# Optimization experiments

Hardware: AMD Instinct MI355X
Metric: run time of the kernel (lower is better)

Reference implementation:

```python
import jax, jax.numpy as jnp
import numpy as np

N = 100000      # nodes
E = 1600000     # edges (avg degree 16)
NFEAT = 16
HID = 64
OUT = 4
K = 3           # TAGConv hops
L = 4           # number of TAGConv layers


def setup_inputs() -> dict:
    key = jax.random.key(0)
    ks = jax.random.split(key, 6)
    x = jax.random.normal(ks[0], (N, NFEAT), dtype=jnp.float32)
    edge_index = jax.random.randint(ks[1], (2, E), 0, N, dtype=jnp.int64)
    # TAGConv has one (bias-free) linear per hop k=0..K, plus a per-layer bias.
    W0 = jax.random.normal(ks[2], (K + 1, NFEAT, HID), dtype=jnp.float32) * 0.1
    b0 = jnp.zeros((HID,), dtype=jnp.float32)
    Wh = jax.random.normal(ks[3], (L - 1, K + 1, HID, HID), dtype=jnp.float32) * 0.1
    bh = jnp.zeros((L - 1, HID), dtype=jnp.float32)
    fcW = jax.random.normal(ks[4], (HID, OUT), dtype=jnp.float32) * 0.1
    fcb = jnp.zeros((OUT,), dtype=jnp.float32)
    return dict(x=x, edge_index=edge_index, W0=W0, b0=b0, Wh=Wh, bh=bh, fcW=fcW, fcb=fcb)


def _gcn_norm(src, dst, num_nodes):
    # symmetric GCN normalization, no self-loops (PyG TAGConv default)
    ones = jnp.ones(src.shape, dtype=jnp.float32)
    deg = jax.ops.segment_sum(ones, dst, num_segments=num_nodes)
    dinv = jnp.where(deg > 0, 1.0 / jnp.sqrt(jnp.maximum(deg, 1e-12)), 0.0)
    return dinv[src] * dinv[dst]  # [E]


def _tag_conv(x, src, dst, norm, W, b):
    # out = sum_{k=0..K} (A_norm^k x) W_k + b
    out = x @ W[0]
    h = x
    for k in range(1, W.shape[0]):
        h = jax.ops.segment_sum(norm[:, None] * h[src], dst, num_segments=x.shape[0])
        out = out + h @ W[k]
    return out + b


def reference(x, edge_index, W0, b0, Wh, bh, fcW, fcb):
    src, dst = edge_index[0], edge_index[1]
    norm = _gcn_norm(src, dst, x.shape[0])
    h = jax.nn.relu(_tag_conv(x, src, dst, norm, W0, b0))  # conv0 (+relu, dropout=identity)
    for l in range(Wh.shape[0] - 1):  # middle convs with relu
        h = jax.nn.relu(_tag_conv(h, src, dst, norm, Wh[l], bh[l]))
    h = _tag_conv(h, src, dst, norm, Wh[-1], bh[-1])  # last conv, no relu
    return h @ fcW + fcb  # [N, OUT]
```

## Files before the change

kernel.cpp:

```cpp
#include <hip/hip_runtime.h>
#include <hip/hip_fp16.h>

constexpr int Nn   = 100000;
constexpr int Ne   = 1600000;
constexpr int NF   = 16;
constexpr int HID  = 64;
constexpr int NOUT = 4;

constexpr int NBUK  = 391;
constexpr int CHUNK = 2048;
constexpr int NB1   = (Ne + CHUNK - 1) / CHUNK;
constexpr int NS    = NBUK * NB1;
constexpr int STASH = 6144;

union H8 { float4 f4; __half h[8]; };
union H4 { float2 f2; __half h[4]; };

typedef _Float16 f16x8 __attribute__((ext_vector_type(8)));
typedef float    f32x4 __attribute__((ext_vector_type(4)));


__global__ __launch_bounds__(256) void bhist_kernel(const int* __restrict__ dst,
                                                    int* __restrict__ ghist) {
    __shared__ int h[NBUK];
    int t = threadIdx.x;
    int b = blockIdx.x;
    for (int i = t; i < NBUK; i += 256) h[i] = 0;
    __syncthreads();
    int e0 = b * CHUNK;
    int e1 = (e0 + CHUNK < Ne) ? e0 + CHUNK : Ne;
    for (int e = e0 + t; e < e1; e += 256) atomicAdd(&h[dst[e] >> 8], 1);
    __syncthreads();
    for (int i = t; i < NBUK; i += 256) ghist[i * NB1 + b] = h[i];
}

__global__ __launch_bounds__(256) void scan1g_kernel(int* __restrict__ g,
                                                     int* __restrict__ bsum) {
    __shared__ int lds[256];
    int t = threadIdx.x;
    int base = blockIdx.x * 1024 + t * 4;
    int v0 = (base + 0 < NS) ? g[base + 0] : 0;
    int v1 = (base + 1 < NS) ? g[base + 1] : 0;
    int v2 = (base + 2 < NS) ? g[base + 2] : 0;
    int v3 = (base + 3 < NS) ? g[base + 3] : 0;
    lds[t] = v0 + v1 + v2 + v3;
    __syncthreads();
    for (int off = 1; off < 256; off <<= 1) {
        int a = lds[t];
        int b = (t >= off) ? lds[t - off] : 0;
        __syncthreads();
        lds[t] = a + b;
        __syncthreads();
    }
    int excl = (t > 0) ? lds[t - 1] : 0;
    if (base + 0 < NS) g[base + 0] = excl;
    if (base + 1 < NS) g[base + 1] = excl + v0;
    if (base + 2 < NS) g[base + 2] = excl + v0 + v1;
    if (base + 3 < NS) g[base + 3] = excl + v0 + v1 + v2;
    if (t == 255) bsum[blockIdx.x] = lds[255];
}

__global__ __launch_bounds__(512) void scan2g_kernel(int* __restrict__ bsum, int nb) {
    __shared__ int lds[512];
    int t = threadIdx.x;
    int v = (t < nb) ? bsum[t] : 0;
    lds[t] = v;
    __syncthreads();
    for (int off = 1; off < 512; off <<= 1) {
        int a = lds[t];
        int b = (t >= off) ? lds[t - off] : 0;
        __syncthreads();
        lds[t] = a + b;
        __syncthreads();
    }
    if (t < nb) bsum[t] = lds[t] - v;
}

__global__ __launch_bounds__(256) void scan3g_kernel(int* __restrict__ g,
                                                     const int* __restrict__ bsum) {
    int i = blockIdx.x * 256 + threadIdx.x;
    if (i < NS) g[i] += bsum[i >> 10];
}

__global__ __launch_bounds__(256) void bscatter_kernel(const int* __restrict__ src,
                                                       const int* __restrict__ dst,
                                                       const int* __restrict__ ghist,
                                                       int2* __restrict__ tmp) {
    __shared__ int hb[NBUK];
    __shared__ int cur[NBUK];
    int t = threadIdx.x;
    int b = blockIdx.x;
    for (int i = t; i < NBUK; i += 256) {
        hb[i] = ghist[i * NB1 + b];
        cur[i] = 0;
    }
    __syncthreads();
    int e0 = b * CHUNK;
    int e1 = (e0 + CHUNK < Ne) ? e0 + CHUNK : Ne;
    for (int e = e0 + t; e < e1; e += 256) {
        int d = dst[e];
        int s = src[e];
        int bin = d >> 8;
        int r = atomicAdd(&cur[bin], 1);
        tmp[hb[bin] + r] = make_int2(s, d);
    }
}

__global__ __launch_bounds__(256) void bcsr_kernel(const int2* __restrict__ tmp,
                                                   const int* __restrict__ ghist,
                                                   int* __restrict__ rowptr,
                                                   float* __restrict__ dinv,
                                                   int* __restrict__ colsrc) {
    __shared__ int2 stash[STASH];
    __shared__ int h[256];
    __shared__ int hs[256];
    __shared__ int cur[256];
    int t = threadIdx.x;
    int b = blockIdx.x;
    int lo = ghist[b * NB1];
    int hi = (b < NBUK - 1) ? ghist[(b + 1) * NB1] : Ne;
    int sz = hi - lo;
    h[t] = 0;
    cur[t] = 0;
    __syncthreads();
    for (int i = t; i < sz; i += 256) {
        int2 rec = tmp[lo + i];
        if (i < STASH) stash[i] = rec;
        atomicAdd(&h[rec.y & 255], 1);
    }
    __syncthreads();
    int myh = h[t];
    hs[t] = myh;
    __syncthreads();
    for (int off = 1; off < 256; off <<= 1) {
        int a = hs[t];
        int bb = (t >= off) ? hs[t - off] : 0;
        __syncthreads();
        hs[t] = a + bb;
        __syncthreads();
    }
    int excl = hs[t] - myh;
    __syncthreads();
    hs[t] = excl;
    int d = (b << 8) + t;
    if (d < Nn) {
        rowptr[d] = lo + excl;
        dinv[d] = (myh > 0) ? rsqrtf((float)myh) : 0.0f;
    }
    if (b == NBUK - 1 && t == 0) rowptr[Nn] = Ne;
    __syncthreads();
    for (int i = t; i < sz; i += 256) {
        int2 rec = (i < STASH) ? stash[i] : tmp[lo + i];
        int bin = rec.y & 255;
        int r = atomicAdd(&cur[bin], 1);
        colsrc[lo + hs[bin] + r] = rec.x;
    }
}

__global__ __launch_bounds__(256) void fill_kernel(const int* __restrict__ colsrc,
                                                   const float* __restrict__ dinv,
                                                   int2* __restrict__ edge2) {
    int e = blockIdx.x * 256 + threadIdx.x;
    if (e < Ne) {
        int s = colsrc[e];
        edge2[e] = make_int2(s, __float_as_int(dinv[s]));
    }
}

__global__ __launch_bounds__(256) void xcvt_kernel(const float* __restrict__ x,
                                                   __half* __restrict__ xh) {
    int i = blockIdx.x * 256 + threadIdx.x;
    if (i < Nn * NF / 4) {
        float4 v = reinterpret_cast<const float4*>(x)[i];
        H4 o;
        o.h[0] = __float2half(v.x);
        o.h[1] = __float2half(v.y);
        o.h[2] = __float2half(v.z);
        o.h[3] = __float2half(v.w);
        reinterpret_cast<float2*>(xh)[i] = o.f2;
    }
}


__global__ __launch_bounds__(256) void pull64h_kernel(const __half* __restrict__ hin,
                                                      const int* __restrict__ rowptr,
                                                      const int2* __restrict__ edge2,
                                                      const float* __restrict__ dinv,
                                                      __half* __restrict__ hout) {
    int lane = threadIdx.x & 63;
    int q  = lane & 3;
    int eo = (lane >> 2) & 3;
    int g  = lane >> 4;
    int n = blockIdx.x * 16 + (threadIdx.x >> 6) * 4 + g;
    if (n >= Nn) return;
    int r0 = rowptr[n];
    int r1 = rowptr[n + 1];
    float a[16];
#pragma unroll
    for (int j = 0; j < 16; ++j) a[j] = 0.f;

    int e = r0 + eo;
    int2 ed0 = (e < r1) ? edge2[e] : make_int2(0, 0);
    int2 ed1 = (e + 4 < r1) ? edge2[e + 4] : make_int2(0, 0);
    const float4* rp0 = reinterpret_cast<const float4*>(hin + (size_t)ed0.x * 64 + q * 16);
    float4 ga = rp0[0], gb = rp0[1];
#pragma unroll 1
    for (; e < r1; e += 4) {
        int2 ed2 = (e + 8 < r1) ? edge2[e + 8] : make_int2(0, 0);
        const float4* rp1 = reinterpret_cast<const float4*>(hin + (size_t)ed1.x * 64 + q * 16);
        float4 na = rp1[0], nb = rp1[1];
        float w = __int_as_float(ed0.y);
        H8 u0, u1;
        u0.f4 = ga;
        u1.f4 = gb;
#pragma unroll
        for (int j = 0; j < 8; ++j) a[j] += w * __half2float(u0.h[j]);
#pragma unroll
        for (int j = 0; j < 8; ++j) a[8 + j] += w * __half2float(u1.h[j]);
        ed0 = ed1; ed1 = ed2; ga = na; gb = nb;
    }
#pragma unroll
    for (int off = 4; off <= 8; off <<= 1)
#pragma unroll
        for (int j = 0; j < 16; ++j) a[j] += __shfl_xor(a[j], off);
    if (eo == 0) {
        float dn = dinv[n];
        H8 o0, o1;
#pragma unroll
        for (int j = 0; j < 8; ++j) o0.h[j] = __float2half(a[j] * dn);
#pragma unroll
        for (int j = 0; j < 8; ++j) o1.h[j] = __float2half(a[8 + j] * dn);
        float4* op = reinterpret_cast<float4*>(hout + (size_t)n * 64 + q * 16);
        op[0] = o0.f4;
        op[1] = o1.f4;
    }
}

__global__ __launch_bounds__(256) void pull16h_kernel(const __half* __restrict__ hin,
                                                      const int* __restrict__ rowptr,
                                                      const int2* __restrict__ edge2,
                                                      const float* __restrict__ dinv,
                                                      __half* __restrict__ hout) {
    int lane = threadIdx.x & 63;
    int q  = lane & 1;
    int eo = (lane >> 1) & 3;
    int g  = lane >> 3;
    int n = blockIdx.x * 32 + (threadIdx.x >> 6) * 8 + g;
    if (n >= Nn) return;
    int r0 = rowptr[n];
    int r1 = rowptr[n + 1];
    float a[8];
#pragma unroll
    for (int j = 0; j < 8; ++j) a[j] = 0.f;

    int e = r0 + eo;
    int2 ed0 = (e < r1) ? edge2[e] : make_int2(0, 0);
    int2 ed1 = (e + 4 < r1) ? edge2[e + 4] : make_int2(0, 0);
    float4 ga = *reinterpret_cast<const float4*>(hin + (size_t)ed0.x * 16 + q * 8);
#pragma unroll 1
    for (; e < r1; e += 4) {
        int2 ed2 = (e + 8 < r1) ? edge2[e + 8] : make_int2(0, 0);
        float4 na = *reinterpret_cast<const float4*>(hin + (size_t)ed1.x * 16 + q * 8);
        float w = __int_as_float(ed0.y);
        H8 u;
        u.f4 = ga;
#pragma unroll
        for (int j = 0; j < 8; ++j) a[j] += w * __half2float(u.h[j]);
        ed0 = ed1; ed1 = ed2; ga = na;
    }
#pragma unroll
    for (int off = 2; off <= 4; off <<= 1)
#pragma unroll
        for (int j = 0; j < 8; ++j) a[j] += __shfl_xor(a[j], off);
    if (eo == 0) {
        float dn = dinv[n];
        H8 o;
#pragma unroll
        for (int j = 0; j < 8; ++j) o.h[j] = __float2half(a[j] * dn);
        *reinterpret_cast<float4*>(hout + (size_t)n * 16 + q * 8) = o.f4;
    }
}

template <int ADDBIAS>
__global__ __launch_bounds__(256) void pull4_kernel(const float* __restrict__ uin,
                                                    const float* __restrict__ gadd,
                                                    const int* __restrict__ rowptr,
                                                    const int2* __restrict__ edge2,
                                                    const float* __restrict__ dinv,
                                                    const float* __restrict__ beff,
                                                    float* __restrict__ out) {
    int lane = threadIdx.x & 63;
    int eo = lane & 15;
    int n = blockIdx.x * 16 + ((threadIdx.x >> 6) << 2) + (lane >> 4);
    if (n >= Nn) return;
    int r0 = rowptr[n];
    int r1 = rowptr[n + 1];
    float ax = 0.f, ay = 0.f, az = 0.f, aw = 0.f;

    int e = r0 + eo;
    int2 ed0 = (e < r1) ? edge2[e] : make_int2(0, 0);
    int2 ed1 = (e + 16 < r1) ? edge2[e + 16] : make_int2(0, 0);
    float4 ga = *reinterpret_cast<const float4*>(uin + (size_t)ed0.x * 4);
#pragma unroll 1
    for (; e < r1; e += 16) {
        int2 ed2 = (e + 32 < r1) ? edge2[e + 32] : make_int2(0, 0);
        float4 na = *reinterpret_cast<const float4*>(uin + (size_t)ed1.x * 4);
        float w = __int_as_float(ed0.y);
        ax += w * ga.x;
        ay += w * ga.y;
        az += w * ga.z;
        aw += w * ga.w;
        ed0 = ed1; ed1 = ed2; ga = na;
    }
#pragma unroll
    for (int off = 1; off < 16; off <<= 1) {
        ax += __shfl_xor(ax, off);
        ay += __shfl_xor(ay, off);
        az += __shfl_xor(az, off);
        aw += __shfl_xor(aw, off);
    }
    if (eo == 0) {
        float dn = dinv[n];
        float4 g = *reinterpret_cast<const float4*>(gadd + (size_t)n * 4);
        float4 o;
        o.x = g.x + dn * ax;
        o.y = g.y + dn * ay;
        o.z = g.z + dn * az;
        o.w = g.w + dn * aw;
        if (ADDBIAS) {
            o.x += beff[0]; o.y += beff[1]; o.z += beff[2]; o.w += beff[3];
        }
        *reinterpret_cast<float4*>(out + (size_t)n * 4) = o;
    }
}

template <int KS>
__global__ __launch_bounds__(256) void wfrag_kernel(const float* __restrict__ W,
                                                    __half* __restrict__ Wfrag) {
    constexpr int NT = (4 * KS / 32) * 4 * 64;
    int tid = blockIdx.x * 256 + threadIdx.x;
    if (tid >= NT) return;
    int l  = tid & 63;
    int ct = (tid >> 6) & 3;
    int ks = tid >> 8;
    int c  = ct * 16 + (l & 15);
    int kb = ks * 32 + (l >> 4) * 8;
    H8 o;
#pragma unroll
    for (int j = 0; j < 8; ++j) {
        int k = kb + j;
        o.h[j] = __float2half(W[(size_t)(k / KS) * KS * 64 + (size_t)(k % KS) * 64 + c]);
    }
    *reinterpret_cast<float4*>(Wfrag + (size_t)tid * 8) = o.f4;
}

template <int KS, int RELU>
__global__ __launch_bounds__(256) void gemm4m_kernel(const __half* __restrict__ S0,
                                                     const __half* __restrict__ S1,
                                                     const __half* __restrict__ S2,
                                                     const __half* __restrict__ S3,
                                                     const __half* __restrict__ Wfrag,
                                                     const float* __restrict__ bias,
                                                     __half* __restrict__ out) {
    constexpr int NKS = 4 * KS / 32;
    int lane = threadIdx.x & 63;
    int wv = threadIdx.x >> 6;
    int base = blockIdx.x * 128 + wv * 32;
    int r = lane & 15;
    int qa = lane >> 4;
    int acol = qa * 8;
    const __half* Ss[4] = {S0, S1, S2, S3};
    f32x4 acc[2][4] = {};
    int row0 = base + r;       if (row0 >= Nn) row0 = Nn - 1;
    int row1 = base + 16 + r;  if (row1 >= Nn) row1 = Nn - 1;
#pragma unroll
    for (int ks = 0; ks < NKS; ++ks) {
        int k0 = ks * 32 + acol;
        const __half* Sa = Ss[k0 / KS];
        int col = k0 % KS;
        f16x8 a0 = *reinterpret_cast<const f16x8*>(Sa + (size_t)row0 * KS + col);
        f16x8 a1 = *reinterpret_cast<const f16x8*>(Sa + (size_t)row1 * KS + col);
        const __half* wp = Wfrag + ((size_t)(ks * 4) * 64 + lane) * 8;
#pragma unroll
        for (int ct = 0; ct < 4; ++ct) {
            f16x8 b = *reinterpret_cast<const f16x8*>(wp + (size_t)ct * 64 * 8);
            acc[0][ct] = __builtin_amdgcn_mfma_f32_16x16x32_f16(a0, b, acc[0][ct], 0, 0, 0);
            acc[1][ct] = __builtin_amdgcn_mfma_f32_16x16x32_f16(a1, b, acc[1][ct], 0, 0, 0);
        }
    }
    int ccol = lane & 15;
    int rb = (lane >> 4) * 4;
#pragma unroll
    for (int rt = 0; rt < 2; ++rt) {
#pragma unroll
        for (int ct = 0; ct < 4; ++ct) {
            float bi = bias[ct * 16 + ccol];
#pragma unroll
            for (int i = 0; i < 4; ++i) {
                int row = base + rt * 16 + rb + i;
                if (row < Nn) {
                    float v = acc[rt][ct][i] + bi;
                    if (RELU) v = fmaxf(v, 0.f);
                    out[(size_t)row * 64 + ct * 16 + ccol] = __float2half(v);
                }
            }
        }
    }
}

__global__ __launch_bounds__(256) void weff_kernel(const float* __restrict__ W,
                                                   const float* __restrict__ b,
                                                   const float* __restrict__ fcW,
                                                   const float* __restrict__ fcb,
                                                   float* __restrict__ Wg,
                                                   float* __restrict__ beff) {
    int t = threadIdx.x;
    int k = t >> 6, c = t & 63;
    const float* wrow = W + (size_t)t * 64;
    float a0 = 0.f, a1 = 0.f, a2 = 0.f, a3 = 0.f;
    for (int d = 0; d < 64; ++d) {
        float w = wrow[d];
        a0 += w * fcW[d * 4 + 0];
        a1 += w * fcW[d * 4 + 1];
        a2 += w * fcW[d * 4 + 2];
        a3 += w * fcW[d * 4 + 3];
    }
    float4 o; o.x = a0; o.y = a1; o.z = a2; o.w = a3;
    *reinterpret_cast<float4*>(Wg + k * 256 + c * 4) = o;
    if (t < 4) {
        float s = fcb[t];
        for (int d = 0; d < 64; ++d) s += b[d] * fcW[d * 4 + t];
        beff[t] = s;
    }
}

__global__ __launch_bounds__(256) void gemmG_kernel(const __half* __restrict__ h,
                                                    const float* __restrict__ Wg,
                                                    float* __restrict__ G) {
    __shared__ float Ht[64 * 65];
    __shared__ float Wl[1024];
    int t = threadIdx.x;
    int r0 = blockIdx.x * 64;
    for (int i = t; i < 256; i += 256)
        *reinterpret_cast<float4*>(&Wl[i * 4]) = *reinterpret_cast<const float4*>(Wg + i * 4);
    for (int i = t; i < 64 * 8; i += 256) {
        int r = i >> 3;
        int c8 = i & 7;
        int row = r0 + r;
        float* hp = &Ht[r * 65 + c8 * 8];
        if (row < Nn) {
            H8 u;
            u.f4 = *reinterpret_cast<const float4*>(h + (size_t)row * 64 + c8 * 8);
#pragma unroll
            for (int j = 0; j < 8; ++j) hp[j] = __half2float(u.h[j]);
        } else {
#pragma unroll
            for (int j = 0; j < 8; ++j) hp[j] = 0.f;
        }
    }
    __syncthreads();
    int r = t & 63;
    int k = t >> 6;
    float a0 = 0.f, a1 = 0.f, a2 = 0.f, a3 = 0.f;
#pragma unroll 8
    for (int c = 0; c < 64; ++c) {
        float hv = Ht[r * 65 + c];
        const float* wp = &Wl[k * 256 + c * 4];
        a0 += hv * wp[0];
        a1 += hv * wp[1];
        a2 += hv * wp[2];
        a3 += hv * wp[3];
    }
    int row = r0 + r;
    if (row < Nn) {
        float4 o; o.x = a0; o.y = a1; o.z = a2; o.w = a3;
        *reinterpret_cast<float4*>(G + (size_t)k * Nn * 4 + (size_t)row * 4) = o;
    }
}


extern "C" void kernel_launch(void* const* d_in, const int* in_sizes, int n_in,
                              void* d_out, int out_size, void* d_ws, size_t ws_size,
                              hipStream_t stream) {
    const float* x   = (const float*)d_in[0];
    const int*   ei  = (const int*)d_in[1];
    const float* W0  = (const float*)d_in[2];
    const float* b0  = (const float*)d_in[3];
    const float* Wh  = (const float*)d_in[4];
    const float* bh  = (const float*)d_in[5];
    const float* fcW = (const float*)d_in[6];
    const float* fcb = (const float*)d_in[7];
    float* out = (float*)d_out;

    const int* src = ei;
    const int* dst = ei + Ne;

    int*    rowptr = (int*)d_ws;
    int2*   edge2  = (int2*)(rowptr + 100004);
    int*    ghist  = (int*)(rowptr + 100004 + 2 * Ne);
    int*    bsum   = ghist + 305792;
    float*  dinv   = (float*)(bsum + 512);
    float*  Wg     = dinv + Nn;
    float*  beff   = Wg + 1024;
    __half* Wf0    = (__half*)(beff + 16);
    __half* Wf1    = Wf0 + 4096;
    __half* Wf2    = Wf1 + 16384;
    __half* xh     = Wf2 + 16384;
    __half* H0     = xh + (size_t)Nn * NF;
    __half* H1     = H0 + (size_t)Nn * HID;
    __half* H2     = H1 + (size_t)Nn * HID;
    __half* H3     = H2 + (size_t)Nn * HID;
    float*  G      = (float*)(H3 + (size_t)Nn * HID);
    float*  G0     = G + 0 * (size_t)Nn * 4;
    float*  G1     = G + 1 * (size_t)Nn * 4;
    float*  G2     = G + 2 * (size_t)Nn * 4;
    float*  G3     = G + 3 * (size_t)Nn * 4;
    float*  T      = G + 4 * (size_t)Nn * 4;
    float*  T2     = G + 5 * (size_t)Nn * 4;
    int2*   tmp    = (int2*)H2;
    int*    colsrc = (int*)H1;

    const int egrid  = (Ne + 255) / 256;
    const int s1grid = (NS + 1023) / 1024;
    const int s3grid = (NS + 255) / 256;
    const int p64grid = (Nn + 15) / 16;
    const int p16grid = (Nn + 31) / 32;
    const int ggrid  = (Nn + 127) / 128;
    const int qgrid  = (Nn + 15) / 16;
    const int Ggrid  = (Nn + 63) / 64;
    const int cgrid  = (Nn * NF / 4 + 255) / 256;

    bhist_kernel<<<NB1, 256, 0, stream>>>(dst, ghist);
    scan1g_kernel<<<s1grid, 256, 0, stream>>>(ghist, bsum);
    scan2g_kernel<<<1, 512, 0, stream>>>(bsum, s1grid);
    scan3g_kernel<<<s3grid, 256, 0, stream>>>(ghist, bsum);
    bscatter_kernel<<<NB1, 256, 0, stream>>>(src, dst, ghist, tmp);
    bcsr_kernel<<<NBUK, 256, 0, stream>>>(tmp, ghist, rowptr, dinv, colsrc);
    fill_kernel<<<egrid, 256, 0, stream>>>(colsrc, dinv, edge2);
    weff_kernel<<<1, 256, 0, stream>>>(Wh + 2 * 4 * 64 * 64, bh + 2 * 64, fcW, fcb, Wg, beff);
    xcvt_kernel<<<cgrid, 256, 0, stream>>>(x, xh);
    wfrag_kernel<16><<<2, 256, 0, stream>>>(W0, Wf0);
    wfrag_kernel<64><<<8, 256, 0, stream>>>(Wh + 0 * 4 * 64 * 64, Wf1);
    wfrag_kernel<64><<<8, 256, 0, stream>>>(Wh + 1 * 4 * 64 * 64, Wf2);

    pull16h_kernel<<<p16grid, 256, 0, stream>>>(xh, rowptr, edge2, dinv, H1);
    pull16h_kernel<<<p16grid, 256, 0, stream>>>(H1, rowptr, edge2, dinv, H2);
    pull16h_kernel<<<p16grid, 256, 0, stream>>>(H2, rowptr, edge2, dinv, H3);
    gemm4m_kernel<16, 1><<<ggrid, 256, 0, stream>>>(xh, H1, H2, H3, Wf0, b0, H0);

    for (int l = 0; l < 2; ++l) {
        pull64h_kernel<<<p64grid, 256, 0, stream>>>(H0, rowptr, edge2, dinv, H1);
        pull64h_kernel<<<p64grid, 256, 0, stream>>>(H1, rowptr, edge2, dinv, H2);
        pull64h_kernel<<<p64grid, 256, 0, stream>>>(H2, rowptr, edge2, dinv, H3);
        gemm4m_kernel<64, 1><<<ggrid, 256, 0, stream>>>(H0, H1, H2, H3,
                                                        (l == 0) ? Wf1 : Wf2,
                                                        bh + (size_t)l * HID, H0);
    }

    gemmG_kernel<<<Ggrid, 256, 0, stream>>>(H0, Wg, G);
    pull4_kernel<0><<<qgrid, 256, 0, stream>>>(G3, G2, rowptr, edge2, dinv, beff, T);
    pull4_kernel<0><<<qgrid, 256, 0, stream>>>(T,  G1, rowptr, edge2, dinv, beff, T2);
    pull4_kernel<1><<<qgrid, 256, 0, stream>>>(T2, G0, rowptr, edge2, dinv, beff, out);
}
```

Before: 506.5 us.

## Split 64-wide SpMM pulls into two feature-half passes with nontemporal edge loads

Each 64-feature propagation is split into two launches, each gathering one 32-feature half (64 bytes per row), so the per-pass working set of gathered features is halved and fits better in cache. Edge (index, weight) pairs are now read with nontemporal 64-bit loads in all pull kernels to avoid polluting cache with streaming data. In exchange, edge lists and rowptr are read twice per hop, and the kernel launch count doubles.

```diff
diff --git a/kernel.cpp b/kernel.cpp
--- a/kernel.cpp
+++ b/kernel.cpp
@@ -18,6 +18,15 @@
 
 typedef _Float16 f16x8 __attribute__((ext_vector_type(8)));
 typedef float    f32x4 __attribute__((ext_vector_type(4)));
+
+#if defined(__has_builtin)
+#if __has_builtin(__builtin_nontemporal_load)
+#define NT_U64(p) __builtin_nontemporal_load((const unsigned long long*)(p))
+#endif
+#endif
+#ifndef NT_U64
+#define NT_U64(p) (*(const unsigned long long*)(p))
+#endif
 
 
 __global__ __launch_bounds__(256) void bhist_kernel(const int* __restrict__ dst,
@@ -182,57 +191,50 @@
 }
 
 
-__global__ __launch_bounds__(256) void pull64h_kernel(const __half* __restrict__ hin,
+__global__ __launch_bounds__(256) void pull64p_kernel(const __half* __restrict__ hin,
                                                       const int* __restrict__ rowptr,
                                                       const int2* __restrict__ edge2,
                                                       const float* __restrict__ dinv,
-                                                      __half* __restrict__ hout) {
+                                                      __half* __restrict__ hout,
+                                                      int plane) {
     int lane = threadIdx.x & 63;
     int q  = lane & 3;
     int eo = (lane >> 2) & 3;
     int g  = lane >> 4;
     int n = blockIdx.x * 16 + (threadIdx.x >> 6) * 4 + g;
     if (n >= Nn) return;
+    const __half* hp = hin + plane * 32 + q * 8;
     int r0 = rowptr[n];
     int r1 = rowptr[n + 1];
-    float a[16];
-#pragma unroll
-    for (int j = 0; j < 16; ++j) a[j] = 0.f;
+    float a[8];
+#pragma unroll
+    for (int j = 0; j < 8; ++j) a[j] = 0.f;
 
     int e = r0 + eo;
-    int2 ed0 = (e < r1) ? edge2[e] : make_int2(0, 0);
-    int2 ed1 = (e + 4 < r1) ? edge2[e + 4] : make_int2(0, 0);
-    const float4* rp0 = reinterpret_cast<const float4*>(hin + (size_t)ed0.x * 64 + q * 16);
-    float4 ga = rp0[0], gb = rp0[1];
+    unsigned long long ed0 = (e < r1) ? NT_U64(&edge2[e]) : 0ull;
+    unsigned long long ed1 = (e + 4 < r1) ? NT_U64(&edge2[e + 4]) : 0ull;
+    float4 ga = *reinterpret_cast<const float4*>(hp + (size_t)(unsigned)(ed0 & 0xffffffffu) * 64);
 #pragma unroll 1
     for (; e < r1; e += 4) {
-        int2 ed2 = (e + 8 < r1) ? edge2[e + 8] : make_int2(0, 0);
-        const float4* rp1 = reinterpret_cast<const float4*>(hin + (size_t)ed1.x * 64 + q * 16);
-        float4 na = rp1[0], nb = rp1[1];
-        float w = __int_as_float(ed0.y);
-        H8 u0, u1;
-        u0.f4 = ga;
-        u1.f4 = gb;
-#pragma unroll
-        for (int j = 0; j < 8; ++j) a[j] += w * __half2float(u0.h[j]);
-#pragma unroll
-        for (int j = 0; j < 8; ++j) a[8 + j] += w * __half2float(u1.h[j]);
-        ed0 = ed1; ed1 = ed2; ga = na; gb = nb;
+        unsigned long long ed2 = (e + 8 < r1) ? NT_U64(&edge2[e + 8]) : 0ull;
+        float4 na = *reinterpret_cast<const float4*>(hp + (size_t)(unsigned)(ed1 & 0xffffffffu) * 64);
+        float w = __int_as_float((int)(ed0 >> 32));
+        H8 u;
+        u.f4 = ga;
+#pragma unroll
+        for (int j = 0; j < 8; ++j) a[j] += w * __half2float(u.h[j]);
+        ed0 = ed1; ed1 = ed2; ga = na;
     }
 #pragma unroll
     for (int off = 4; off <= 8; off <<= 1)
 #pragma unroll
-        for (int j = 0; j < 16; ++j) a[j] += __shfl_xor(a[j], off);
+        for (int j = 0; j < 8; ++j) a[j] += __shfl_xor(a[j], off);
     if (eo == 0) {
         float dn = dinv[n];
-        H8 o0, o1;
-#pragma unroll
-        for (int j = 0; j < 8; ++j) o0.h[j] = __float2half(a[j] * dn);
-#pragma unroll
-        for (int j = 0; j < 8; ++j) o1.h[j] = __float2half(a[8 + j] * dn);
-        float4* op = reinterpret_cast<float4*>(hout + (size_t)n * 64 + q * 16);
-        op[0] = o0.f4;
-        op[1] = o1.f4;
+        H8 o;
+#pragma unroll
+        for (int j = 0; j < 8; ++j) o.h[j] = __float2half(a[j] * dn);
+        *reinterpret_cast<float4*>(hout + (size_t)n * 64 + plane * 32 + q * 8) = o.f4;
     }
 }
 
@@ -254,14 +256,14 @@
     for (int j = 0; j < 8; ++j) a[j] = 0.f;
 
     int e = r0 + eo;
-    int2 ed0 = (e < r1) ? edge2[e] : make_int2(0, 0);
-    int2 ed1 = (e + 4 < r1) ? edge2[e + 4] : make_int2(0, 0);
-    float4 ga = *reinterpret_cast<const float4*>(hin + (size_t)ed0.x * 16 + q * 8);
+    unsigned long long ed0 = (e < r1) ? NT_U64(&edge2[e]) : 0ull;
+    unsigned long long ed1 = (e + 4 < r1) ? NT_U64(&edge2[e + 4]) : 0ull;
+    float4 ga = *reinterpret_cast<const float4*>(hin + (size_t)(unsigned)(ed0 & 0xffffffffu) * 16 + q * 8);
 #pragma unroll 1
     for (; e < r1; e += 4) {
-        int2 ed2 = (e + 8 < r1) ? edge2[e + 8] : make_int2(0, 0);
-        float4 na = *reinterpret_cast<const float4*>(hin + (size_t)ed1.x * 16 + q * 8);
-        float w = __int_as_float(ed0.y);
+        unsigned long long ed2 = (e + 8 < r1) ? NT_U64(&edge2[e + 8]) : 0ull;
+        float4 na = *reinterpret_cast<const float4*>(hin + (size_t)(unsigned)(ed1 & 0xffffffffu) * 16 + q * 8);
+        float w = __int_as_float((int)(ed0 >> 32));
         H8 u;
         u.f4 = ga;
 #pragma unroll
@@ -298,14 +300,14 @@
     float ax = 0.f, ay = 0.f, az = 0.f, aw = 0.f;
 
     int e = r0 + eo;
-    int2 ed0 = (e < r1) ? edge2[e] : make_int2(0, 0);
-    int2 ed1 = (e + 16 < r1) ? edge2[e + 16] : make_int2(0, 0);
-    float4 ga = *reinterpret_cast<const float4*>(uin + (size_t)ed0.x * 4);
+    unsigned long long ed0 = (e < r1) ? NT_U64(&edge2[e]) : 0ull;
+    unsigned long long ed1 = (e + 16 < r1) ? NT_U64(&edge2[e + 16]) : 0ull;
+    float4 ga = *reinterpret_cast<const float4*>(uin + (size_t)(unsigned)(ed0 & 0xffffffffu) * 4);
 #pragma unroll 1
     for (; e < r1; e += 16) {
-        int2 ed2 = (e + 32 < r1) ? edge2[e + 32] : make_int2(0, 0);
-        float4 na = *reinterpret_cast<const float4*>(uin + (size_t)ed1.x * 4);
-        float w = __int_as_float(ed0.y);
+        unsigned long long ed2 = (e + 32 < r1) ? NT_U64(&edge2[e + 32]) : 0ull;
+        float4 na = *reinterpret_cast<const float4*>(uin + (size_t)(unsigned)(ed1 & 0xffffffffu) * 4);
+        float w = __int_as_float((int)(ed0 >> 32));
         ax += w * ga.x;
         ay += w * ga.y;
         az += w * ga.z;
@@ -549,9 +551,12 @@
     gemm4m_kernel<16, 1><<<ggrid, 256, 0, stream>>>(xh, H1, H2, H3, Wf0, b0, H0);
 
     for (int l = 0; l < 2; ++l) {
-        pull64h_kernel<<<p64grid, 256, 0, stream>>>(H0, rowptr, edge2, dinv, H1);
-        pull64h_kernel<<<p64grid, 256, 0, stream>>>(H1, rowptr, edge2, dinv, H2);
-        pull64h_kernel<<<p64grid, 256, 0, stream>>>(H2, rowptr, edge2, dinv, H3);
+        pull64p_kernel<<<p64grid, 256, 0, stream>>>(H0, rowptr, edge2, dinv, H1, 0);
+        pull64p_kernel<<<p64grid, 256, 0, stream>>>(H0, rowptr, edge2, dinv, H1, 1);
+        pull64p_kernel<<<p64grid, 256, 0, stream>>>(H1, rowptr, edge2, dinv, H2, 0);
+        pull64p_kernel<<<p64grid, 256, 0, stream>>>(H1, rowptr, edge2, dinv, H2, 1);
+        pull64p_kernel<<<p64grid, 256, 0, stream>>>(H2, rowptr, edge2, dinv, H3, 0);
+        pull64p_kernel<<<p64grid, 256, 0, stream>>>(H2, rowptr, edge2, dinv, H3, 1);
         gemm4m_kernel<64, 1><<<ggrid, 256, 0, stream>>>(H0, H1, H2, H3,
                                                         (l == 0) ? Wf1 : Wf2,
                                                         bh + (size_t)l * HID, H0);
```

After: 749.5 us. +48.0%, slower.
